# Optimization experiments

Measured on AMD Instinct MI355X. Metric: run time of the kernel, lower is better.

Reference implementation:

```python
import jax, jax.numpy as jnp
import numpy as np

KPS = 39
EPS = 1e-05

def _prelu(h, a):
    return jnp.where(h >= 0, h, a * h)

def _ln(h, alpha, beta):
    mean = jnp.mean(h, axis=-1, keepdims=True)
    var = jnp.mean((h - mean) ** 2, axis=-1, keepdims=True)
    return (h - mean) / jnp.sqrt(var + EPS) * alpha + beta

def setup_inputs() -> dict:
    key = jax.random.key(0)
    ks = jax.random.split(key, 8)
    B, T = 256, 2048
    d_in, d_hid = 2 * KPS, 5 * KPS  # 78, 195
    # xavier_uniform with gain for relu = sqrt(2)
    def xavier(k, shape):
        fan_out, fan_in = shape
        gain = np.sqrt(2.0)
        bound = gain * np.sqrt(6.0 / (fan_in + fan_out))
        return jax.random.uniform(k, shape, jnp.float32, -bound, bound)
    return {
        "x": jax.random.normal(ks[0], (B, T, KPS), jnp.float32),
        "y": jax.random.normal(ks[1], (B, T, KPS), jnp.float32),
        "W1": xavier(ks[2], (d_hid, d_in)),   # [195, 78]
        "b1": jnp.zeros((d_hid,), jnp.float32),
        "W2": xavier(ks[3], (d_in, d_hid)),   # [78, 195]
        "b2": jnp.zeros((d_in,), jnp.float32),
        "a1": jnp.full((1,), 0.25, jnp.float32),  # PReLU default
        "a2": jnp.full((1,), 0.25, jnp.float32),
        "alpha1": jnp.ones((d_hid,), jnp.float32),
        "beta1": jnp.zeros((d_hid,), jnp.float32),
        "alpha2": jnp.ones((d_in,), jnp.float32),
        "beta2": jnp.zeros((d_in,), jnp.float32),
    }

def reference(x, y, W1, b1, W2, b2, a1, a2, alpha1, beta1, alpha2, beta2):
    joined = jnp.concatenate((x, y), axis=-1)        # [B, T, 78]
    h = jnp.einsum('btd,hd->bth', joined, W1) + b1   # [B, T, 195]
    h = _ln(_prelu(h, a1), alpha1, beta1)
    # dropout p=0.1 is identity in eval mode
    h = jnp.einsum('bth,dh->btd', h, W2) + b2        # [B, T, 78]
    h = _ln(_prelu(h, a2), alpha2, beta2)
    out = h + joined
    return out[..., :KPS], out[..., KPS:]
```

## Files before the change

### kernel.cpp

```cpp
#include <hip/hip_runtime.h>
#include <hip/hip_bf16.h>

typedef unsigned short u16;
typedef unsigned int   u32;

#define KPS     39
#define DIN     78
#define DHID    195
#define NTOKTOT (256*2048)

#define S1      104
#define M1T     13
#define K1S     3
#define M2T     5
#define K2S     7
#define NW      12
#define NTHR    (NW*64)
#define TPI     (NW*16)
#define TPB     2048
#define FIT     10
#define NBLK    (NTOKTOT/TPB)

#define W1F_E (M1T*K1S*64*8)
#define W2F_E (M2T*K2S*64*8)
#define JND_E (TPI*S1)
#define SMEM_BYTES ((W1F_E+W2F_E+JND_E)*2 + DIN*2*4 + DIN*4)

typedef __attribute__((ext_vector_type(8))) short short8;
typedef __attribute__((ext_vector_type(4))) float float4v;
typedef __attribute__((ext_vector_type(4))) u32   uint4v;

static __device__ __forceinline__ u16 f2b(float v) {
  __hip_bfloat16 b = __float2bfloat16(v);
  return __builtin_bit_cast(u16, b);
}
static __device__ __forceinline__ float b2f(u16 u) {
  return __builtin_bit_cast(float, ((u32)u) << 16);
}

extern "C" __global__
__attribute__((amdgpu_flat_work_group_size(NTHR, NTHR), amdgpu_waves_per_eu(3, 3)))
void fused_mlp_kernel(const float* __restrict__ xp,  const float* __restrict__ yp,
                      const float* __restrict__ W1p, const float* __restrict__ b1p,
                      const float* __restrict__ W2p, const float* __restrict__ b2p,
                      const float* __restrict__ a1p, const float* __restrict__ a2p,
                      const float* __restrict__ al1p,const float* __restrict__ be1p,
                      const float* __restrict__ al2p,const float* __restrict__ be2p,
                      float* __restrict__ out0, float* __restrict__ out1)
{
  extern __shared__ char smem[];
  u16*   W1F = (u16*)smem;
  u16*   W2F = W1F + W1F_E;
  u16*   JND = W2F + W2F_E;
  float* AB2 = (float*)(JND + JND_E);
  float* B2C = AB2 + DIN*2;

  const int tid  = threadIdx.x;
  const int lane = tid & 63;
  const int w    = tid >> 6;
  const int c    = lane & 15;
  const int quad = lane >> 4;
  const int wr   = w * 16;
  const int blockTok = blockIdx.x * TPB;

  float4v xr0, xr1, xr2, yr0, yr1, yr2;
  {
    const float4v* xw = (const float4v*)(xp + (size_t)(blockTok + wr) * KPS);
    const float4v* yw = (const float4v*)(yp + (size_t)(blockTok + wr) * KPS);
    xr0 = xw[lane];      yr0 = yw[lane];
    xr1 = xw[lane + 64]; yr1 = yw[lane + 64];
    if (lane < 28) { xr2 = xw[lane + 128]; yr2 = yw[lane + 128]; }
    else { xr2 = (float4v)0.f; yr2 = (float4v)0.f; }
  }

  {
    float* SCR = (float*)JND;
    if (tid < DIN*4) {
      int d = tid >> 2, p = tid & 3;
      float s = (p == 0) ? b2p[d] : 0.f;
      const float* wrow = W2p + d*DHID;
      for (int j = p; j < DHID; j += 4) s = __builtin_fmaf(wrow[j], be1p[j], s);
      SCR[tid] = s;
    }
  }
  __syncthreads();
  if (tid < DIN) {
    const float* SCR = (const float*)JND;
    B2C[tid] = SCR[4*tid] + SCR[4*tid+1] + SCR[4*tid+2] + SCR[4*tid+3];
    AB2[2*tid+0] = al2p[tid];
    AB2[2*tid+1] = be2p[tid];
  }
  for (int s = tid; s < M1T*K1S*64; s += NTHR) {
    int m = s/(K1S*64), r = s - m*(K1S*64);
    int kt = r >> 6, l = r & 63;
    int cc = l & 15, qq = l >> 4;
    int row = m*16 + cc, k0 = kt*32 + qq*8;
    short8 v;
    #pragma unroll
    for (int e = 0; e < 8; ++e) {
      int k = k0 + e; float f = 0.f;
      if (row < DHID) { if (k < DIN) f = W1p[row*DIN + k]; else if (k == DIN) f = b1p[row]; }
      v[e] = (short)f2b(f);
    }
    *(short8*)&W1F[(size_t)s*8] = v;
  }
  __syncthreads();
  for (int s = tid; s < M2T*K2S*64; s += NTHR) {
    int m = s/(K2S*64), r = s - m*(K2S*64);
    int kt = r >> 6, l = r & 63;
    int cc = l & 15, qq = l >> 4;
    int d = m*16 + cc;
    short8 v;
    #pragma unroll
    for (int e = 0; e < 8; ++e) {
      int k = kt*32 + (e>>2)*16 + qq*4 + (e&3);
      float f = 0.f;
      if (d < DIN) {
        if (k < DHID)       f = W2p[d*DHID + k] * al1p[k];
        else if (k == DHID) f = B2C[d];
      }
      v[e] = (short)f2b(f);
    }
    *(short8*)&W2F[(size_t)s*8] = v;
  }
  for (int i = tid; i < TPI*18; i += NTHR) {
    int t = i/18, cf = i - t*18;
    JND[t*S1 + DIN + cf] = (cf == 0) ? (u16)0x3F80 : (u16)0;
  }
  __syncthreads();

  const float a1v = a1p[0];
  const float a2v = a2p[0];

  int joff[12];
  #pragma unroll
  for (int s = 0; s < 3; ++s) {
    int i4 = lane + s*64;
    #pragma unroll
    for (int k = 0; k < 4; ++k) {
      int idx = i4*4 + k;
      int t = idx / KPS, cc2 = idx - t*KPS;
      joff[s*4+k] = (wr + t)*S1 + cc2;
    }
  }

  const u16* pW1 = W1F + (size_t)lane*8;
  const u16* pW2 = W2F + (size_t)lane*8;
  u16* pJ = JND + (wr + c)*S1;

  #pragma unroll 1
  for (int it = 0; it <= FIT; ++it) {
    const int tb = blockTok + it * TPI;
    const bool active = (it < FIT) || (w < 8);

    if (active) {
      #pragma unroll
      for (int k = 0; k < 4; ++k) {
        JND[joff[k]]         = f2b(xr0[k]);
        JND[joff[k] + KPS]   = f2b(yr0[k]);
        JND[joff[4+k]]       = f2b(xr1[k]);
        JND[joff[4+k] + KPS] = f2b(yr1[k]);
      }
      if (lane < 28) {
        #pragma unroll
        for (int k = 0; k < 4; ++k) {
          JND[joff[8+k]]       = f2b(xr2[k]);
          JND[joff[8+k] + KPS] = f2b(yr2[k]);
        }
      }
    }

    if (it < FIT) {
      const bool pact = (it + 1 < FIT) || (w < 8);
      if (pact) {
        const float4v* xw = (const float4v*)(xp + (size_t)(tb + TPI + wr) * KPS);
        const float4v* yw = (const float4v*)(yp + (size_t)(tb + TPI + wr) * KPS);
        xr0 = xw[lane];      yr0 = yw[lane];
        xr1 = xw[lane + 64]; yr1 = yw[lane + 64];
        if (lane < 28) { xr2 = xw[lane + 128]; yr2 = yw[lane + 128]; }
      }
    }

    if (!active) continue;

    float4v acc1[M1T];
    #pragma unroll
    for (int m = 0; m < M1T; ++m)
      #pragma unroll
      for (int q = 0; q < 4; ++q) acc1[m][q] = 0.f;

    #pragma unroll
    for (int kt = 0; kt < K1S; ++kt) {
      short8 bfr = *(const short8*)&pJ[kt*32 + quad*8];
      #pragma unroll
      for (int m = 0; m < M1T; ++m) {
        short8 afr = *(const short8*)&pW1[(m*K1S + kt)*512];
        acc1[m] = __builtin_amdgcn_mfma_f32_16x16x32_bf16(afr, bfr, acc1[m], 0, 0, 0);
      }
    }

    float sum = 0.f, ss = 0.f;
    #pragma unroll
    for (int m = 0; m < M1T; ++m)
      #pragma unroll
      for (int q = 0; q < 4; ++q) {
        float h = acc1[m][q];
        float p = fmaxf(h, 0.f) + a1v * fminf(h, 0.f);
        acc1[m][q] = p;
        sum += p;
        ss = __builtin_fmaf(p, p, ss);
      }
    sum += __shfl_xor(sum, 16, 64);
    sum += __shfl_xor(sum, 32, 64);
    ss  += __shfl_xor(ss,  16, 64);
    ss  += __shfl_xor(ss,  32, 64);
    const float mean = sum * (1.f/DHID);
    const float istd = rsqrtf(ss*(1.f/DHID) - mean*mean + 1e-5f);

    u32 pn[26];
    #pragma unroll
    for (int m = 0; m < 12; ++m) {
      u16 p0 = f2b((acc1[m][0] - mean)*istd);
      u16 p1 = f2b((acc1[m][1] - mean)*istd);
      u16 p2 = f2b((acc1[m][2] - mean)*istd);
      u16 p3 = f2b((acc1[m][3] - mean)*istd);
      pn[2*m]   = (u32)p0 | ((u32)p1 << 16);
      pn[2*m+1] = (u32)p2 | ((u32)p3 << 16);
    }
    {
      float n0 = (quad == 0) ? (acc1[12][0] - mean)*istd : 0.f;
      float n1 = (quad == 0) ? (acc1[12][1] - mean)*istd : 0.f;
      float n2 = (quad == 0) ? (acc1[12][2] - mean)*istd : 0.f;
      u16 pb = (quad == 0) ? (u16)0x3F80 : (u16)0;
      pn[24] = (u32)f2b(n0) | ((u32)f2b(n1) << 16);
      pn[25] = (u32)f2b(n2) | ((u32)pb    << 16);
    }

    float4v acc2[M2T];
    #pragma unroll
    for (int m = 0; m < M2T; ++m)
      #pragma unroll
      for (int q = 0; q < 4; ++q) acc2[m][q] = 0.f;

    #pragma unroll
    for (int kt = 0; kt < K2S; ++kt) {
      uint4v bu;
      bu[0] = pn[4*kt + 0];
      bu[1] = pn[4*kt + 1];
      bu[2] = (kt < 6) ? pn[4*kt + 2] : 0u;
      bu[3] = (kt < 6) ? pn[4*kt + 3] : 0u;
      short8 bfr = __builtin_bit_cast(short8, bu);
      #pragma unroll
      for (int m = 0; m < M2T; ++m) {
        short8 afr = *(const short8*)&pW2[(m*K2S + kt)*512];
        acc2[m] = __builtin_amdgcn_mfma_f32_16x16x32_bf16(afr, bfr, acc2[m], 0, 0, 0);
      }
    }

    float sum2 = 0.f, ss2 = 0.f;
    #pragma unroll
    for (int m = 0; m < M2T; ++m)
      #pragma unroll
      for (int q = 0; q < 4; ++q) {
        float h = acc2[m][q];
        float p = fmaxf(h, 0.f) + a2v * fminf(h, 0.f);
        acc2[m][q] = p;
        sum2 += p;
        ss2 = __builtin_fmaf(p, p, ss2);
      }
    sum2 += __shfl_xor(sum2, 16, 64);
    sum2 += __shfl_xor(sum2, 32, 64);
    ss2  += __shfl_xor(ss2,  16, 64);
    ss2  += __shfl_xor(ss2,  32, 64);
    const float mean2 = sum2 * (1.f/DIN);
    const float istd2 = rsqrtf(ss2*(1.f/DIN) - mean2*mean2 + 1e-5f);

    const int gt = tb + wr + c;
    #pragma unroll
    for (int m = 0; m < M2T; ++m) {
      int d0 = m*16 + quad*4;
      if (d0 < DIN) {
        ushort4 res = *(const ushort4*)&pJ[d0];
        u16 rr[4] = {res.x, res.y, res.z, res.w};
        #pragma unroll
        for (int r = 0; r < 4; ++r) {
          int d = d0 + r;
          if (d < DIN) {
            float2 ab = *(const float2*)&AB2[2*d];
            float  v  = (acc2[m][r] - mean2)*istd2*ab.x + ab.y + b2f(rr[r]);
            if (d < KPS) out0[(size_t)gt*KPS + d]         = v;
            else         out1[(size_t)gt*KPS + (d - KPS)] = v;
          }
        }
      }
    }
  }
}

extern "C" void kernel_launch(void* const* d_in, const int* in_sizes, int n_in,
                              void* d_out, int out_size, void* d_ws, size_t ws_size,
                              hipStream_t stream) {
  const float* xp   = (const float*)d_in[0];
  const float* yp   = (const float*)d_in[1];
  const float* W1p  = (const float*)d_in[2];
  const float* b1p  = (const float*)d_in[3];
  const float* W2p  = (const float*)d_in[4];
  const float* b2p  = (const float*)d_in[5];
  const float* a1p  = (const float*)d_in[6];
  const float* a2p  = (const float*)d_in[7];
  const float* al1p = (const float*)d_in[8];
  const float* be1p = (const float*)d_in[9];
  const float* al2p = (const float*)d_in[10];
  const float* be2p = (const float*)d_in[11];

  float* out0 = (float*)d_out;
  float* out1 = out0 + (size_t)NTOKTOT * KPS;

  hipFuncSetAttribute((const void*)fused_mlp_kernel,
                      hipFuncAttributeMaxDynamicSharedMemorySize, SMEM_BYTES);

  fused_mlp_kernel<<<NBLK, NTHR, SMEM_BYTES, stream>>>(
      xp, yp, W1p, b1p, W2p, b2p, a1p, a2p, al1p, be1p, al2p, be2p, out0, out1);
}
```

Measured before the change: 368.2 us.

## Stage x/y tiles via global_load_lds as fp32 and convert fragments on read

Each wave now loads its 16-token x and y tiles straight from global memory into LDS in fp32 with global_load_lds. The MFMA B fragments are built from that buffer and converted to bf16 at read time, and W1 is repacked to match the split x/y layout. This removes the register round-trip and the scattered bf16 scatter-stores into a padded joined buffer, and the residual add now uses full-precision inputs. In exchange, the loads no longer prefetch the next iteration: each iteration waits on vmcnt(0) before compute, which exposes global latency. LDS use for the input tile also doubles.

```diff
diff --git a/kernel.cpp b/kernel.cpp
--- a/kernel.cpp
+++ b/kernel.cpp
@@ -9,7 +9,6 @@
 #define DHID    195
 #define NTOKTOT (256*2048)
 
-#define S1      104
 #define M1T     13
 #define K1S     3
 #define M2T     5
@@ -23,8 +22,8 @@
 
 #define W1F_E (M1T*K1S*64*8)
 #define W2F_E (M2T*K2S*64*8)
-#define JND_E (TPI*S1)
-#define SMEM_BYTES ((W1F_E+W2F_E+JND_E)*2 + DIN*2*4 + DIN*4)
+#define XYB_F (NW*1248)
+#define SMEM_BYTES ((W1F_E+W2F_E)*2 + XYB_F*4 + DIN*2*4 + DIN*4)
 
 typedef __attribute__((ext_vector_type(8))) short short8;
 typedef __attribute__((ext_vector_type(4))) float float4v;
@@ -34,8 +33,11 @@
   __hip_bfloat16 b = __float2bfloat16(v);
   return __builtin_bit_cast(u16, b);
 }
-static __device__ __forceinline__ float b2f(u16 u) {
-  return __builtin_bit_cast(float, ((u32)u) << 16);
+
+static __device__ __forceinline__ void glds16(const float* g, float* l) {
+  __builtin_amdgcn_global_load_lds((const __attribute__((address_space(1))) void*)g,
+                                   (__attribute__((address_space(3))) void*)l,
+                                   16, 0, 0);
 }
 
 extern "C" __global__
@@ -51,8 +53,8 @@
   extern __shared__ char smem[];
   u16*   W1F = (u16*)smem;
   u16*   W2F = W1F + W1F_E;
-  u16*   JND = W2F + W2F_E;
-  float* AB2 = (float*)(JND + JND_E);
+  float* XYB = (float*)(W2F + W2F_E);
+  float* AB2 = XYB + XYB_F;
   float* B2C = AB2 + DIN*2;
 
   const int tid  = threadIdx.x;
@@ -63,18 +65,8 @@
   const int wr   = w * 16;
   const int blockTok = blockIdx.x * TPB;
 
-  float4v xr0, xr1, xr2, yr0, yr1, yr2;
   {
-    const float4v* xw = (const float4v*)(xp + (size_t)(blockTok + wr) * KPS);
-    const float4v* yw = (const float4v*)(yp + (size_t)(blockTok + wr) * KPS);
-    xr0 = xw[lane];      yr0 = yw[lane];
-    xr1 = xw[lane + 64]; yr1 = yw[lane + 64];
-    if (lane < 28) { xr2 = xw[lane + 128]; yr2 = yw[lane + 128]; }
-    else { xr2 = (float4v)0.f; yr2 = (float4v)0.f; }
-  }
-
-  {
-    float* SCR = (float*)JND;
+    float* SCR = XYB;
     if (tid < DIN*4) {
       int d = tid >> 2, p = tid & 3;
       float s = (p == 0) ? b2p[d] : 0.f;
@@ -85,26 +77,38 @@
   }
   __syncthreads();
   if (tid < DIN) {
-    const float* SCR = (const float*)JND;
-    B2C[tid] = SCR[4*tid] + SCR[4*tid+1] + SCR[4*tid+2] + SCR[4*tid+3];
+    const float* SCR = XYB;
+    float bsum = SCR[4*tid] + SCR[4*tid+1] + SCR[4*tid+2] + SCR[4*tid+3];
+    B2C[tid] = bsum;
     AB2[2*tid+0] = al2p[tid];
     AB2[2*tid+1] = be2p[tid];
   }
+  __syncthreads();
   for (int s = tid; s < M1T*K1S*64; s += NTHR) {
     int m = s/(K1S*64), r = s - m*(K1S*64);
     int kt = r >> 6, l = r & 63;
     int cc = l & 15, qq = l >> 4;
-    int row = m*16 + cc, k0 = kt*32 + qq*8;
+    int row = m*16 + cc;
     short8 v;
     #pragma unroll
     for (int e = 0; e < 8; ++e) {
-      int k = k0 + e; float f = 0.f;
-      if (row < DHID) { if (k < DIN) f = W1p[row*DIN + k]; else if (k == DIN) f = b1p[row]; }
+      float f = 0.f;
+      if (row < DHID) {
+        int k = -1;
+        if (kt == 0)      k = qq*8 + e;
+        else if (kt == 1) k = (qq == 0) ? ((e < 7) ? 32 + e : -1)
+                                        : 39 + (qq-1)*8 + e;
+        else {
+          if (qq == 0)      k = 63 + e;
+          else if (qq == 1) k = (e < 7) ? 71 + e : -1;
+          else if (qq == 2 && e == 0) f = b1p[row];
+        }
+        if (k >= 0) f = W1p[row*DIN + k];
+      }
       v[e] = (short)f2b(f);
     }
     *(short8*)&W1F[(size_t)s*8] = v;
   }
-  __syncthreads();
   for (int s = tid; s < M2T*K2S*64; s += NTHR) {
     int m = s/(K2S*64), r = s - m*(K2S*64);
     int kt = r >> 6, l = r & 63;
@@ -123,75 +127,75 @@
     }
     *(short8*)&W2F[(size_t)s*8] = v;
   }
-  for (int i = tid; i < TPI*18; i += NTHR) {
-    int t = i/18, cf = i - t*18;
-    JND[t*S1 + DIN + cf] = (cf == 0) ? (u16)0x3F80 : (u16)0;
-  }
   __syncthreads();
 
   const float a1v = a1p[0];
   const float a2v = a2p[0];
 
-  int joff[12];
-  #pragma unroll
-  for (int s = 0; s < 3; ++s) {
-    int i4 = lane + s*64;
-    #pragma unroll
-    for (int k = 0; k < 4; ++k) {
-      int idx = i4*4 + k;
-      int t = idx / KPS, cc2 = idx - t*KPS;
-      joff[s*4+k] = (wr + t)*S1 + cc2;
-    }
-  }
-
   const u16* pW1 = W1F + (size_t)lane*8;
   const u16* pW2 = W2F + (size_t)lane*8;
-  u16* pJ = JND + (wr + c)*S1;
+  float* XB = XYB + w*1248;
+  float* YB = XB + 624;
+  const float* xrow = XB + c*39;
+  const float* yrow = YB + c*39;
 
   #pragma unroll 1
   for (int it = 0; it <= FIT; ++it) {
+    if (it == FIT && w >= 8) break;
     const int tb = blockTok + it * TPI;
-    const bool active = (it < FIT) || (w < 8);
-
-    if (active) {
-      #pragma unroll
-      for (int k = 0; k < 4; ++k) {
-        JND[joff[k]]         = f2b(xr0[k]);
-        JND[joff[k] + KPS]   = f2b(yr0[k]);
-        JND[joff[4+k]]       = f2b(xr1[k]);
-        JND[joff[4+k] + KPS] = f2b(yr1[k]);
-      }
+
+    asm volatile("s_waitcnt lgkmcnt(0)" ::: "memory");
+    __builtin_amdgcn_sched_barrier(0);
+    {
+      const float* xg = xp + (size_t)(tb + wr) * KPS;
+      const float* yg = yp + (size_t)(tb + wr) * KPS;
+      glds16(xg + (size_t)lane*4,         XB);
+      glds16(xg + (size_t)(64+lane)*4,    XB + 256);
+      glds16(yg + (size_t)lane*4,         YB);
+      glds16(yg + (size_t)(64+lane)*4,    YB + 256);
       if (lane < 28) {
+        glds16(xg + (size_t)(128+lane)*4, XB + 512);
+        glds16(yg + (size_t)(128+lane)*4, YB + 512);
+      }
+    }
+    asm volatile("s_waitcnt vmcnt(0)" ::: "memory");
+    __builtin_amdgcn_sched_barrier(0);
+
+    float4v acc1[M1T];
+    #pragma unroll
+    for (int m = 0; m < M1T; ++m)
+      #pragma unroll
+      for (int q = 0; q < 4; ++q) acc1[m][q] = 0.f;
+
+    #pragma unroll
+    for (int kt = 0; kt < K1S; ++kt) {
+      float bv[8];
+      if (kt == 0) {
+        const float* p = xrow + quad*8;
         #pragma unroll
-        for (int k = 0; k < 4; ++k) {
-          JND[joff[8+k]]       = f2b(xr2[k]);
-          JND[joff[8+k] + KPS] = f2b(yr2[k]);
+        for (int e = 0; e < 8; ++e) bv[e] = p[e];
+      } else if (kt == 1) {
+        const float* p = (quad == 0) ? (xrow + 32) : (yrow + (quad-1)*8);
+        #pragma unroll
+        for (int e = 0; e < 8; ++e) bv[e] = p[e];
+        if (quad == 0) bv[7] = 0.f;
+      } else {
+        if (quad < 2) {
+          const float* p = (quad == 0) ? (yrow + 24) : (yrow + 32);
+          #pragma unroll
+          for (int e = 0; e < 8; ++e) bv[e] = p[e];
+          if (quad == 1) bv[7] = 0.f;
+        } else {
+          #pragma unroll
+          for (int e = 0; e < 8; ++e) bv[e] = 0.f;
+          if (quad == 2) bv[0] = 1.f;
         }
       }
-    }
-
-    if (it < FIT) {
-      const bool pact = (it + 1 < FIT) || (w < 8);
-      if (pact) {
-        const float4v* xw = (const float4v*)(xp + (size_t)(tb + TPI + wr) * KPS);
-        const float4v* yw = (const float4v*)(yp + (size_t)(tb + TPI + wr) * KPS);
-        xr0 = xw[lane];      yr0 = yw[lane];
-        xr1 = xw[lane + 64]; yr1 = yw[lane + 64];
-        if (lane < 28) { xr2 = xw[lane + 128]; yr2 = yw[lane + 128]; }
-      }
-    }
-
-    if (!active) continue;
-
-    float4v acc1[M1T];
-    #pragma unroll
-    for (int m = 0; m < M1T; ++m)
-      #pragma unroll
-      for (int q = 0; q < 4; ++q) acc1[m][q] = 0.f;
-
-    #pragma unroll
-    for (int kt = 0; kt < K1S; ++kt) {
-      short8 bfr = *(const short8*)&pJ[kt*32 + quad*8];
+      uint4v bu;
+      #pragma unroll
+      for (int j = 0; j < 4; ++j)
+        bu[j] = (u32)f2b(bv[2*j]) | ((u32)f2b(bv[2*j+1]) << 16);
+      short8 bfr = __builtin_bit_cast(short8, bu);
       #pragma unroll
       for (int m = 0; m < M1T; ++m) {
         short8 afr = *(const short8*)&pW1[(m*K1S + kt)*512];
@@ -279,18 +283,15 @@
     #pragma unroll
     for (int m = 0; m < M2T; ++m) {
       int d0 = m*16 + quad*4;
-      if (d0 < DIN) {
-        ushort4 res = *(const ushort4*)&pJ[d0];
-        u16 rr[4] = {res.x, res.y, res.z, res.w};
-        #pragma unroll
-        for (int r = 0; r < 4; ++r) {
-          int d = d0 + r;
-          if (d < DIN) {
-            float2 ab = *(const float2*)&AB2[2*d];
-            float  v  = (acc2[m][r] - mean2)*istd2*ab.x + ab.y + b2f(rr[r]);
-            if (d < KPS) out0[(size_t)gt*KPS + d]         = v;
-            else         out1[(size_t)gt*KPS + (d - KPS)] = v;
-          }
+      #pragma unroll
+      for (int r = 0; r < 4; ++r) {
+        int d = d0 + r;
+        if (d < DIN) {
+          float res = (d < KPS) ? xrow[d] : yrow[d - KPS];
+          float2 ab = *(const float2*)&AB2[2*d];
+          float  v  = (acc2[m][r] - mean2)*istd2*ab.x + ab.y + res;
+          if (d < KPS) out0[(size_t)gt*KPS + d]         = v;
+          else         out1[(size_t)gt*KPS + (d - KPS)] = v;
         }
       }
     }
```

Result: no change. 375.1 us (+1.9%).
